# Kernel optimization log

Hardware: AMD Instinct MI355X
Metric: run time of the kernel (lower is better)

## Reference

```python
import jax, jax.numpy as jnp
import numpy as np


def _nms(heat, kernel=3):
    # 3x3 max-pool, stride 1, SAME padding; keep only local maxima
    pad = (kernel - 1) // 2
    hmax = jax.lax.reduce_window(
        heat, -jnp.inf, jax.lax.max,
        window_dimensions=(1, 1, kernel, kernel),
        window_strides=(1, 1, 1, 1),
        padding=((0, 0), (0, 0), (pad, pad), (pad, pad)))
    keep = (hmax == heat).astype(heat.dtype)
    return heat * keep


def _topk(scores, K):
    b, c, h, w = scores.shape
    # stage 1: per-class top-K over spatial positions
    topk_scores, topk_inds = jax.lax.top_k(scores.reshape(b, c, h * w), K)  # [b,c,K]
    topk_inds = topk_inds % (h * w)
    topk_ys = (topk_inds // w).astype(scores.dtype)
    topk_xs = (topk_inds % w).astype(scores.dtype)
    # stage 2: global top-K over the c*K per-class candidates
    topk_score, topk_ind = jax.lax.top_k(topk_scores.reshape(b, c * K), K)  # [b,K]
    topk_clses = (topk_ind // K).astype(jnp.int32)
    gather = lambda f: jnp.take_along_axis(f.reshape(b, c * K), topk_ind, axis=1)
    return (topk_score, gather(topk_inds), topk_clses, gather(topk_ys), gather(topk_xs))


def setup_inputs() -> dict:
    key = jax.random.key(0)
    heat = jax.random.uniform(key, (8, 10, 512, 512), dtype=jnp.float32)
    return {"heat": heat, "K": 100}


def reference(heat, K):
    suppressed = _nms(heat, kernel=3)
    return _topk(suppressed, K)
```

## Files before the change

kernel.cpp:

```cpp
#include <hip/hip_runtime.h>
#include <cstdint>

using u32 = unsigned int;
using u64 = unsigned long long;

#define WDIM 512
#define HDIM 512
#define CHANNELS 80
#define SELBINS 4096
#define SORTN 2048
#define TOPK 100
#define NEG_SENTINEL -1e30f
#define CNT_STRIDE 16

__device__ __forceinline__ float fmax3(float a, float b, float c) {
  return fmaxf(fmaxf(a, b), c);
}

__device__ __forceinline__ int key_bin(u64 key) {
  int b = (int)((u32)(key >> 32) >> 14) - 60928;
  return b < 0 ? 0 : b;
}

struct H8 { float h0, h1, h2, h3, h4, h5, h6, h7; };
struct Row { float l; float4 A; float4 B; float r; };

__device__ __forceinline__ Row load_row_shfl(const float* __restrict__ chbase,
                                             int y, int x0) {
  Row o;
  if (y >= 0 && y < HDIM) {
    const float* row = chbase + (size_t)y * WDIM;
    o.A = *reinterpret_cast<const float4*>(row + x0);
    o.B = *reinterpret_cast<const float4*>(row + x0 + 4);
  } else {
    o.A = make_float4(NEG_SENTINEL, NEG_SENTINEL, NEG_SENTINEL, NEG_SENTINEL);
    o.B = o.A;
  }
  o.l = __shfl_up(o.B.w, 1);
  o.r = __shfl_down(o.A.x, 1);
  int lane = threadIdx.x & 63;
  if (lane == 0) o.l = NEG_SENTINEL;
  if (lane == 63) o.r = NEG_SENTINEL;
  return o;
}

__device__ __forceinline__ H8 hmax_row(const Row& t) {
  H8 o;
  o.h0 = fmax3(t.l,   t.A.x, t.A.y);
  o.h1 = fmax3(t.A.x, t.A.y, t.A.z);
  o.h2 = fmax3(t.A.y, t.A.z, t.A.w);
  o.h3 = fmax3(t.A.z, t.A.w, t.B.x);
  o.h4 = fmax3(t.A.w, t.B.x, t.B.y);
  o.h5 = fmax3(t.B.x, t.B.y, t.B.z);
  o.h6 = fmax3(t.B.y, t.B.z, t.B.w);
  o.h7 = fmax3(t.B.z, t.B.w, t.r);
  return o;
}

__global__ __launch_bounds__(256) void nms_collect_all(
    const float* __restrict__ heat, u64* __restrict__ keys_all,
    u32* __restrict__ cnt, int cap_all) {
  const int ch = blockIdx.y;
  const float* chbase = heat + (size_t)ch * (WDIM * HDIM);
  __shared__ u32 lcnt, lbase;
  __shared__ u64 lk[2048];
  if (threadIdx.x == 0) lcnt = 0;
  __syncthreads();

  const int P = blockIdx.x * 2048 + threadIdx.x * 8;
  const int y = P >> 9, x0 = P & 511;
  Row rt = load_row_shfl(chbase, y - 1, x0);
  Row rm = load_row_shfl(chbase, y,     x0);
  Row rb = load_row_shfl(chbase, y + 1, x0);
  H8 ht = hmax_row(rt), hm = hmax_row(rm), hb = hmax_row(rb);

#define DO_PIX(I, VC, HT, HM, HB)                                         \
  {                                                                       \
    float v = (VC);                                                       \
    if (v == fmax3((HT), (HM), (HB)) && v > 0.0f) {                       \
      u32 p = atomicAdd(&lcnt, 1u);                                       \
      lk[p] = ((u64)__float_as_uint(v) << 32) | (u32)(~(u32)(P + (I)));   \
    }                                                                     \
  }
  DO_PIX(0, rm.A.x, ht.h0, hm.h0, hb.h0)
  DO_PIX(1, rm.A.y, ht.h1, hm.h1, hb.h1)
  DO_PIX(2, rm.A.z, ht.h2, hm.h2, hb.h2)
  DO_PIX(3, rm.A.w, ht.h3, hm.h3, hb.h3)
  DO_PIX(4, rm.B.x, ht.h4, hm.h4, hb.h4)
  DO_PIX(5, rm.B.y, ht.h5, hm.h5, hb.h5)
  DO_PIX(6, rm.B.z, ht.h6, hm.h6, hb.h6)
  DO_PIX(7, rm.B.w, ht.h7, hm.h7, hb.h7)
#undef DO_PIX

  __syncthreads();
  if (threadIdx.x == 0) lbase = atomicAdd(&cnt[ch * CNT_STRIDE], lcnt);
  __syncthreads();
  const u32 n = lcnt, base = lbase;
  u64* dst = keys_all + (size_t)ch * cap_all;
  for (u32 i = threadIdx.x; i < n; i += 256) {
    u32 pos = base + i;
    if (pos < (u32)cap_all) dst[pos] = lk[i];
  }
}

__device__ __forceinline__ void bitonic_desc(u64* keys, int N, int nthr, int tid) {
  for (unsigned size = 2; size <= (unsigned)N; size <<= 1) {
    for (unsigned stride = size >> 1; stride > 0; stride >>= 1) {
      __syncthreads();
      for (unsigned i = tid; i < (unsigned)N; i += nthr) {
        unsigned j = i ^ stride;
        if (j > i) {
          u64 a = keys[i], b = keys[j];
          bool desc = ((i & size) == 0);
          if ((a < b) == desc) { keys[i] = b; keys[j] = a; }
        }
      }
    }
  }
  __syncthreads();
}

__global__ __launch_bounds__(1024) void select_kernel(
    const u64* __restrict__ keys_all, const u32* __restrict__ cnt, int cap_all,
    float* __restrict__ s1s, int* __restrict__ s1i) {
  const int ch = blockIdx.x;
  const u64* keys = keys_all + (size_t)ch * cap_all;
  const int n = min((int)cnt[ch * CNT_STRIDE], cap_all);

  __shared__ u32 hist[SELBINS];
  __shared__ u64 sk[SORTN];
  __shared__ int sT;
  __shared__ u32 scand;

  for (int i = threadIdx.x; i < SELBINS; i += 1024) hist[i] = 0;
  if (threadIdx.x == 0) scand = 0;
  __syncthreads();

  for (int i = threadIdx.x; i < n; i += 1024)
    atomicAdd(&hist[key_bin(keys[i])], 1u);
  __syncthreads();

  if (threadIdx.x == 0) {
    u32 cum = 0;
    int b = SELBINS - 1;
    for (; b >= 0; b--) {
      cum += hist[b];
      if (cum >= TOPK) break;
    }
    sT = b < 0 ? 0 : b;
  }
  __syncthreads();
  const int T = sT;

  for (int i = threadIdx.x; i < n; i += 1024) {
    u64 k = keys[i];
    if (key_bin(k) >= T) {
      u32 p = atomicAdd(&scand, 1u);
      if (p < SORTN) sk[p] = k;
    }
  }
  __syncthreads();
  const int nc = min((int)scand, SORTN);
  for (int i = threadIdx.x; i < SORTN; i += 1024)
    if (i >= nc) sk[i] = 0;
  bitonic_desc(sk, SORTN, 1024, threadIdx.x);

  for (int k = threadIdx.x; k < TOPK; k += 1024) {
    u64 key = sk[k];
    s1s[ch * TOPK + k] = __uint_as_float((u32)(key >> 32));
    s1i[ch * TOPK + k] = (int)(~(u32)key);
  }
}

__global__ __launch_bounds__(256) void batch_topk_kernel(
    const float* __restrict__ s1s, const int* __restrict__ s1i,
    float* __restrict__ out) {
  const int b = blockIdx.x;
  __shared__ u64 keys[1024];
  for (int i = threadIdx.x; i < 1024; i += 256) {
    u64 k = 0;
    if (i < 1000) {
      u32 vb = __float_as_uint(s1s[b * 1000 + i]);
      k = ((u64)vb << 32) | (u32)(~(u32)i);
    }
    keys[i] = k;
  }
  bitonic_desc(keys, 1024, 256, threadIdx.x);
  for (int k = threadIdx.x; k < TOPK; k += 256) {
    u64 key = keys[k];
    float sc = __uint_as_float((u32)(key >> 32));
    int flat = (int)(~(u32)key);
    int cls = flat / 100;
    int spatial = s1i[b * 1000 + flat];
    out[0 * 800 + b * TOPK + k] = sc;
    out[1 * 800 + b * TOPK + k] = (float)spatial;
    out[2 * 800 + b * TOPK + k] = (float)cls;
    out[3 * 800 + b * TOPK + k] = (float)(spatial >> 9);
    out[4 * 800 + b * TOPK + k] = (float)(spatial & 511);
  }
}

extern "C" void kernel_launch(void* const* d_in, const int* in_sizes, int n_in,
                              void* d_out, int out_size, void* d_ws, size_t ws_size,
                              hipStream_t stream) {
  const float* heat = (const float*)d_in[0];
  char* ws = (char*)d_ws;
  float* out = (float*)d_out;

  int cap_all = 49152;
  {
    size_t fixed = (size_t)CHANNELS * CNT_STRIDE * 4 + 4096 + CHANNELS * TOPK * 8;
    while (cap_all > 16384 &&
           fixed + (size_t)CHANNELS * cap_all * 8 > ws_size)
      cap_all >>= 1;
  }

  size_t p = 0;
  u32* cnt      = (u32*)(ws + p); p += (size_t)CHANNELS * CNT_STRIDE * 4;
  const size_t zero_bytes = p;
  p = (p + 255) & ~(size_t)255;
  u64* keys_all = (u64*)(ws + p); p += (size_t)CHANNELS * cap_all * 8;
  float* s1s    = (float*)(ws + p); p += CHANNELS * TOPK * 4;
  int*   s1i    = (int*)  (ws + p); p += CHANNELS * TOPK * 4;

  hipMemsetAsync(d_ws, 0, zero_bytes, stream);

  dim3 nms_grid(128, CHANNELS);
  nms_collect_all<<<nms_grid, 256, 0, stream>>>(heat, keys_all, cnt, cap_all);
  select_kernel<<<CHANNELS, 1024, 0, stream>>>(keys_all, cnt, cap_all, s1s, s1i);
  batch_topk_kernel<<<8, 256, 0, stream>>>(s1s, s1i, out);
}
```

Baseline: 197.7 us.

## Fuse NMS with per-strip top-K selection and add per-channel merge kernel

Replaces the global key-collection pass and per-channel select kernel with a fused kernel. Each block handles a 64-row strip of one channel, keeps surviving peaks in shared memory, and selects that strip's top-K locally with a histogram threshold and a 512-element bitonic sort. A new merge kernel combines the 8 strip results per channel. This removes the global key buffer round-trip, the memset, and the underutilised 80-block select stage. Each wave now walks 8 rows with rolling row reuse, which cuts redundant row loads. The trade-offs are fewer, larger blocks with heavy shared memory use, a possible key overflow beyond 4096 per strip, and a truncated candidate set beyond 512.

New measurement: 188.4 us. -4.7%, faster.

```diff
diff --git a/kernel.cpp b/kernel.cpp
--- a/kernel.cpp
+++ b/kernel.cpp
@@ -7,11 +7,13 @@
 #define WDIM 512
 #define HDIM 512
 #define CHANNELS 80
-#define SELBINS 4096
-#define SORTN 2048
+#define NSTRIP 8
+#define STRIPROWS 64
+#define KEYCAP 4096
+#define HBINS 4096
+#define SORTA 512
 #define TOPK 100
 #define NEG_SENTINEL -1e30f
-#define CNT_STRIDE 16
 
 __device__ __forceinline__ float fmax3(float a, float b, float c) {
   return fmaxf(fmaxf(a, b), c);
@@ -55,52 +57,6 @@
   o.h6 = fmax3(t.B.y, t.B.z, t.B.w);
   o.h7 = fmax3(t.B.z, t.B.w, t.r);
   return o;
-}
-
-__global__ __launch_bounds__(256) void nms_collect_all(
-    const float* __restrict__ heat, u64* __restrict__ keys_all,
-    u32* __restrict__ cnt, int cap_all) {
-  const int ch = blockIdx.y;
-  const float* chbase = heat + (size_t)ch * (WDIM * HDIM);
-  __shared__ u32 lcnt, lbase;
-  __shared__ u64 lk[2048];
-  if (threadIdx.x == 0) lcnt = 0;
-  __syncthreads();
-
-  const int P = blockIdx.x * 2048 + threadIdx.x * 8;
-  const int y = P >> 9, x0 = P & 511;
-  Row rt = load_row_shfl(chbase, y - 1, x0);
-  Row rm = load_row_shfl(chbase, y,     x0);
-  Row rb = load_row_shfl(chbase, y + 1, x0);
-  H8 ht = hmax_row(rt), hm = hmax_row(rm), hb = hmax_row(rb);
-
-#define DO_PIX(I, VC, HT, HM, HB)                                         \
-  {                                                                       \
-    float v = (VC);                                                       \
-    if (v == fmax3((HT), (HM), (HB)) && v > 0.0f) {                       \
-      u32 p = atomicAdd(&lcnt, 1u);                                       \
-      lk[p] = ((u64)__float_as_uint(v) << 32) | (u32)(~(u32)(P + (I)));   \
-    }                                                                     \
-  }
-  DO_PIX(0, rm.A.x, ht.h0, hm.h0, hb.h0)
-  DO_PIX(1, rm.A.y, ht.h1, hm.h1, hb.h1)
-  DO_PIX(2, rm.A.z, ht.h2, hm.h2, hb.h2)
-  DO_PIX(3, rm.A.w, ht.h3, hm.h3, hb.h3)
-  DO_PIX(4, rm.B.x, ht.h4, hm.h4, hb.h4)
-  DO_PIX(5, rm.B.y, ht.h5, hm.h5, hb.h5)
-  DO_PIX(6, rm.B.z, ht.h6, hm.h6, hb.h6)
-  DO_PIX(7, rm.B.w, ht.h7, hm.h7, hb.h7)
-#undef DO_PIX
-
-  __syncthreads();
-  if (threadIdx.x == 0) lbase = atomicAdd(&cnt[ch * CNT_STRIDE], lcnt);
-  __syncthreads();
-  const u32 n = lcnt, base = lbase;
-  u64* dst = keys_all + (size_t)ch * cap_all;
-  for (u32 i = threadIdx.x; i < n; i += 256) {
-    u32 pos = base + i;
-    if (pos < (u32)cap_all) dst[pos] = lk[i];
-  }
 }
 
 __device__ __forceinline__ void bitonic_desc(u64* keys, int N, int nthr, int tid) {
@@ -120,29 +76,68 @@
   __syncthreads();
 }
 
-__global__ __launch_bounds__(1024) void select_kernel(
-    const u64* __restrict__ keys_all, const u32* __restrict__ cnt, int cap_all,
-    float* __restrict__ s1s, int* __restrict__ s1i) {
-  const int ch = blockIdx.x;
-  const u64* keys = keys_all + (size_t)ch * cap_all;
-  const int n = min((int)cnt[ch * CNT_STRIDE], cap_all);
-
-  __shared__ u32 hist[SELBINS];
-  __shared__ u64 sk[SORTN];
+__global__ __launch_bounds__(512) void nms_topk_strip(
+    const float* __restrict__ heat, u64* __restrict__ s1p) {
+  const int strip = blockIdx.x, ch = blockIdx.y;
+  const float* chbase = heat + (size_t)ch * (WDIM * HDIM);
+
+  __shared__ u64 keys[KEYCAP];
+  __shared__ u32 hist[HBINS];
+  __shared__ u64 sk[SORTA];
+  __shared__ u32 lcnt, scand;
   __shared__ int sT;
-  __shared__ u32 scand;
-
-  for (int i = threadIdx.x; i < SELBINS; i += 1024) hist[i] = 0;
-  if (threadIdx.x == 0) scand = 0;
-  __syncthreads();
-
-  for (int i = threadIdx.x; i < n; i += 1024)
+
+  for (int i = threadIdx.x; i < HBINS; i += 512) hist[i] = 0;
+  if (threadIdx.x == 0) { lcnt = 0; scand = 0; }
+  __syncthreads();
+
+  const int lane = threadIdx.x & 63;
+  const int wave = threadIdx.x >> 6;
+  const int x0 = lane * 8;
+  const int yb = strip * STRIPROWS + wave * 8;
+
+  Row rm = load_row_shfl(chbase, yb, x0);
+  H8 ht = hmax_row(load_row_shfl(chbase, yb - 1, x0));
+  H8 hm = hmax_row(rm);
+
+  for (int j = 0; j < 8; j++) {
+    const int y = yb + j;
+    Row rb = load_row_shfl(chbase, y + 1, x0);
+    H8 hb = hmax_row(rb);
+    const int P = (y << 9) + x0;
+
+#define DO_PIX(I, VC, HX)                                                  \
+    {                                                                      \
+      float v = (VC);                                                      \
+      if (v == fmax3(ht.HX, hm.HX, hb.HX) && v > 0.0f) {                   \
+        u32 p = atomicAdd(&lcnt, 1u);                                      \
+        if (p < KEYCAP)                                                    \
+          keys[p] = ((u64)__float_as_uint(v) << 32) | (u32)(~(u32)(P + (I))); \
+      }                                                                    \
+    }
+    DO_PIX(0, rm.A.x, h0)
+    DO_PIX(1, rm.A.y, h1)
+    DO_PIX(2, rm.A.z, h2)
+    DO_PIX(3, rm.A.w, h3)
+    DO_PIX(4, rm.B.x, h4)
+    DO_PIX(5, rm.B.y, h5)
+    DO_PIX(6, rm.B.z, h6)
+    DO_PIX(7, rm.B.w, h7)
+#undef DO_PIX
+
+    rm = rb; ht = hm; hm = hb;
+  }
+
+  __syncthreads();
+  const int n = min((int)lcnt, KEYCAP);
+
+  for (int i = threadIdx.x; i < n; i += 512)
     atomicAdd(&hist[key_bin(keys[i])], 1u);
   __syncthreads();
 
   if (threadIdx.x == 0) {
     u32 cum = 0;
-    int b = SELBINS - 1;
+    int b = HBINS - 1;
     for (; b >= 0; b--) {
       cum += hist[b];
       if (cum >= TOPK) break;
@@ -152,46 +147,55 @@
   __syncthreads();
   const int T = sT;
 
-  for (int i = threadIdx.x; i < n; i += 1024) {
+  for (int i = threadIdx.x; i < n; i += 512) {
     u64 k = keys[i];
     if (key_bin(k) >= T) {
       u32 p = atomicAdd(&scand, 1u);
-      if (p < SORTN) sk[p] = k;
-    }
-  }
-  __syncthreads();
-  const int nc = min((int)scand, SORTN);
-  for (int i = threadIdx.x; i < SORTN; i += 1024)
+      if (p < SORTA) sk[p] = k;
+    }
+  }
+  __syncthreads();
+  const int nc = min((int)scand, SORTA);
+  for (int i = threadIdx.x; i < SORTA; i += 512)
     if (i >= nc) sk[i] = 0;
-  bitonic_desc(sk, SORTN, 1024, threadIdx.x);
-
-  for (int k = threadIdx.x; k < TOPK; k += 1024) {
-    u64 key = sk[k];
-    s1s[ch * TOPK + k] = __uint_as_float((u32)(key >> 32));
-    s1i[ch * TOPK + k] = (int)(~(u32)key);
-  }
+  bitonic_desc(sk, SORTA, 512, threadIdx.x);
+
+  u64* dst = s1p + ((size_t)ch * NSTRIP + strip) * TOPK;
+  for (int k = threadIdx.x; k < TOPK; k += 512) dst[k] = sk[k];
+}
+
+__global__ __launch_bounds__(256) void merge_channel(
+    const u64* __restrict__ s1p, u64* __restrict__ chtop) {
+  const int ch = blockIdx.x;
+  __shared__ u64 sk[1024];
+  const u64* src = s1p + (size_t)ch * NSTRIP * TOPK;
+  for (int i = threadIdx.x; i < 1024; i += 256)
+    sk[i] = (i < NSTRIP * TOPK) ? src[i] : 0;
+  bitonic_desc(sk, 1024, 256, threadIdx.x);
+  for (int k = threadIdx.x; k < TOPK; k += 256)
+    chtop[(size_t)ch * TOPK + k] = sk[k];
 }
 
 __global__ __launch_bounds__(256) void batch_topk_kernel(
-    const float* __restrict__ s1s, const int* __restrict__ s1i,
-    float* __restrict__ out) {
+    const u64* __restrict__ chtop, float* __restrict__ out) {
   const int b = blockIdx.x;
-  __shared__ u64 keys[1024];
+  __shared__ u64 sk[1024];
+  const u64* base = chtop + (size_t)b * 10 * TOPK;
   for (int i = threadIdx.x; i < 1024; i += 256) {
     u64 k = 0;
     if (i < 1000) {
-      u32 vb = __float_as_uint(s1s[b * 1000 + i]);
+      u32 vb = (u32)(base[i] >> 32);
       k = ((u64)vb << 32) | (u32)(~(u32)i);
     }
-    keys[i] = k;
-  }
-  bitonic_desc(keys, 1024, 256, threadIdx.x);
+    sk[i] = k;
+  }
+  bitonic_desc(sk, 1024, 256, threadIdx.x);
   for (int k = threadIdx.x; k < TOPK; k += 256) {
-    u64 key = keys[k];
+    u64 key = sk[k];
     float sc = __uint_as_float((u32)(key >> 32));
     int flat = (int)(~(u32)key);
     int cls = flat / 100;
-    int spatial = s1i[b * 1000 + flat];
+    int spatial = (int)(~(u32)(base[flat]));
     out[0 * 800 + b * TOPK + k] = sc;
     out[1 * 800 + b * TOPK + k] = (float)spatial;
     out[2 * 800 + b * TOPK + k] = (float)cls;
@@ -207,26 +211,12 @@
   char* ws = (char*)d_ws;
   float* out = (float*)d_out;
 
-  int cap_all = 49152;
-  {
-    size_t fixed = (size_t)CHANNELS * CNT_STRIDE * 4 + 4096 + CHANNELS * TOPK * 8;
-    while (cap_all > 16384 &&
-           fixed + (size_t)CHANNELS * cap_all * 8 > ws_size)
-      cap_all >>= 1;
-  }
-
   size_t p = 0;
-  u32* cnt      = (u32*)(ws + p); p += (size_t)CHANNELS * CNT_STRIDE * 4;
-  const size_t zero_bytes = p;
-  p = (p + 255) & ~(size_t)255;
-  u64* keys_all = (u64*)(ws + p); p += (size_t)CHANNELS * cap_all * 8;
-  float* s1s    = (float*)(ws + p); p += CHANNELS * TOPK * 4;
-  int*   s1i    = (int*)  (ws + p); p += CHANNELS * TOPK * 4;
-
-  hipMemsetAsync(d_ws, 0, zero_bytes, stream);
-
-  dim3 nms_grid(128, CHANNELS);
-  nms_collect_all<<<nms_grid, 256, 0, stream>>>(heat, keys_all, cnt, cap_all);
-  select_kernel<<<CHANNELS, 1024, 0, stream>>>(keys_all, cnt, cap_all, s1s, s1i);
-  batch_topk_kernel<<<8, 256, 0, stream>>>(s1s, s1i, out);
-}
+  u64* s1p   = (u64*)(ws + p); p += (size_t)CHANNELS * NSTRIP * TOPK * 8;
+  u64* chtop = (u64*)(ws + p); p += (size_t)CHANNELS * TOPK * 8;
+
+  dim3 gridA(NSTRIP, CHANNELS);
+  nms_topk_strip<<<gridA, 512, 0, stream>>>(heat, s1p);
+  merge_channel<<<CHANNELS, 256, 0, stream>>>(s1p, chtop);
+  batch_topk_kernel<<<8, 256, 0, stream>>>(chtop, out);
+}
```
